# Kernel tuning notes

Hardware: AMD Instinct MI355X
Metric: run time of the kernel (lower is better)

The kernel has to match this reference:

```python
import jax, jax.numpy as jnp
import numpy as np

B, N_PER, H, EMB, V, S, L = 128, 205, 200, 768, 50265, 512, 6
N = B * N_PER

def conv1d(x, w, b, pad):
    # x: [B, Cin, L], w: [Cout, Cin, K]
    out = jax.lax.conv_general_dilated(x, w, (1,), [(pad, pad)],
                                       dimension_numbers=('NCH', 'OIH', 'NCH'))
    return out + b[None, :, None]

def setup_inputs() -> dict:
    key = jax.random.key(0)
    ks = jax.random.split(key, 24)
    s = lambda fan: 1.0 / np.sqrt(fan)
    inp = {
        'x': jax.random.normal(ks[0], (N, H), jnp.float32),
        'edge_index': jax.random.randint(ks[1], (2, 209920), 0, N, jnp.int32),
        'input_ids': jax.random.randint(ks[2], (B, S), 0, V, jnp.int32),
        'embed_table': jax.random.normal(ks[3], (V, EMB), jnp.float32) * 0.02,
        'ggc_w': jax.random.normal(ks[4], (L, H, H), jnp.float32) * s(H),
        'gru_wih': jax.random.normal(ks[5], (3 * H, H), jnp.float32) * s(H),
        'gru_whh': jax.random.normal(ks[6], (3 * H, H), jnp.float32) * s(H),
        'gru_bih': jnp.zeros((3 * H,), jnp.float32),
        'gru_bhh': jnp.zeros((3 * H,), jnp.float32),
        'conv0_w': jax.random.normal(ks[7], (200, 200, 3), jnp.float32) * s(200 * 3),
        'conv0_b': jnp.zeros((200,), jnp.float32),
        'conv1_w': jax.random.normal(ks[8], (200, EMB, 3), jnp.float32) * s(EMB * 3),
        'conv1_b': jnp.zeros((200,), jnp.float32),
        'conv2_w': jax.random.normal(ks[9], (200, EMB, 4), jnp.float32) * s(EMB * 4),
        'conv2_b': jnp.zeros((200,), jnp.float32),
        'conv3_w': jax.random.normal(ks[10], (200, EMB, 5), jnp.float32) * s(EMB * 5),
        'conv3_b': jnp.zeros((200,), jnp.float32),
        'fc1_w': jax.random.normal(ks[11], (256, 800), jnp.float32) * s(800),
        'fc1_b': jnp.zeros((256,), jnp.float32),
        'fc2_w': jax.random.normal(ks[12], (128, 256), jnp.float32) * s(256),
        'fc2_b': jnp.zeros((128,), jnp.float32),
        'fc3_w': jax.random.normal(ks[13], (2, 128), jnp.float32) * s(128),
        'fc3_b': jnp.zeros((2,), jnp.float32),
    }
    return inp

def gated_graph_conv(x, edge_index, ggc_w, wih, whh, bih, bhh):
    src, dst = edge_index[0], edge_index[1]
    h = x  # [N, H], in_dim == out_channels so no padding needed
    for i in range(L):
        m = h @ ggc_w[i]                                   # [N, H]
        agg = jax.ops.segment_sum(m[src], dst, num_segments=N)  # scatter-add at targets
        gi = agg @ wih.T + bih                             # [N, 3H]
        gh = h @ whh.T + bhh
        ir, iz, inn = jnp.split(gi, 3, axis=1)
        hr, hz, hn = jnp.split(gh, 3, axis=1)
        r = jax.nn.sigmoid(ir + hr)
        z = jax.nn.sigmoid(iz + hz)
        n = jnp.tanh(inn + r * hn)
        h = (1.0 - z) * n + z * h
    return h

def reference(x, edge_index, input_ids, embed_table, ggc_w, gru_wih, gru_whh,
              gru_bih, gru_bhh, conv0_w, conv0_b, conv1_w, conv1_b, conv2_w,
              conv2_b, conv3_w, conv3_b, fc1_w, fc1_b, fc2_w, fc2_b, fc3_w, fc3_b):
    g = gated_graph_conv(x, edge_index, ggc_w, gru_wih, gru_whh, gru_bih, gru_bhh)
    g = g.reshape(B, N_PER, H).transpose(0, 2, 1)          # [B, 200, N_PER]
    e = embed_table[input_ids].transpose(0, 2, 1)          # [B, 768, S]
    x0 = jax.nn.relu(conv1d(g, conv0_w, conv0_b, 1))
    x1 = jax.nn.relu(conv1d(e, conv1_w, conv1_b, 0))
    x2 = jax.nn.relu(conv1d(e, conv2_w, conv2_b, 0))
    x3 = jax.nn.relu(conv1d(e, conv3_w, conv3_b, 0))
    feats = jnp.concatenate([x0.max(axis=2), x1.max(axis=2),
                             x2.max(axis=2), x3.max(axis=2)], axis=1)  # [B, 800]
    h = jax.nn.relu(feats @ fc1_w.T + fc1_b)   # dropout is identity in eval
    h = jax.nn.relu(h @ fc2_w.T + fc2_b)
    return h @ fc3_w.T + fc3_b                 # [B, 2]
```

## Files before the change

### kernel.cpp

```cpp
#include <hip/hip_runtime.h>
#include <math.h>

namespace {

constexpr int NB    = 128;
constexpr int NPER  = 205;
constexpr int H     = 200;
constexpr int EMBD  = 768;
constexpr int SEQ   = 512;
constexpr int NLAY  = 6;
constexpr int NNODE = NB * NPER;
constexpr int NEDGE = 209920;
constexpr int KP    = 448;
constexpr int HOFF  = 224;

typedef __bf16 bf16;
typedef _Float16 f16;
typedef __attribute__((ext_vector_type(8))) __bf16 bf16x8;
typedef __attribute__((ext_vector_type(8))) _Float16 f16x8;
typedef __attribute__((ext_vector_type(4))) float f32x4;
typedef unsigned short ushort8 __attribute__((ext_vector_type(8)));
typedef float float4v __attribute__((ext_vector_type(4)));

__device__ __forceinline__ float sigm(float x) { return 1.0f / (1.0f + expf(-x)); }

__device__ __forceinline__ unsigned short f2bf(float x) {
    unsigned int u = __float_as_uint(x);
    unsigned int r = (u + 0x7fffu + ((u >> 16) & 1u)) >> 16;
    return (unsigned short)r;
}
__device__ __forceinline__ unsigned short f2h(float x) {
    union { f16 h; unsigned short u; } c;
    c.h = (f16)x;
    return c.u;
}
__device__ __forceinline__ float h2f(unsigned short u) {
    union { unsigned short u; f16 h; } c;
    c.u = u;
    return (float)c.h;
}

__device__ __forceinline__ int pk_unit(int row, int s) {
    int q = row >> 1;
    return q * 8 + ((((row & 1) << 2) | s) ^ (q & 7));
}

template<bool BIAS, bool OUTF16>
__global__ __launch_bounds__(256, 4)
void gemm_w64(const unsigned short* __restrict__ A, int lda,
              const unsigned short* __restrict__ B, size_t strideBz,
              const float* __restrict__ bias, int Mreal, int Nreal,
              float* __restrict__ Cf, unsigned short* __restrict__ Ch, size_t strideCz,
              int ldc, int Kpad)
{
    __shared__ unsigned short As[128 * 64];
    __shared__ unsigned short Bs[128 * 64];

    const int p0 = blockIdx.x * 128;
    const int o0 = blockIdx.y * 128;
    const unsigned short* Bz = B + (size_t)blockIdx.z * strideBz;
    const int tid = threadIdx.x, lane = tid & 63, wid = tid >> 6;
    const int wm = wid >> 1, wn = wid & 1;
    const int lrow = lane & 15, lk = lane >> 4;

    f32x4 acc[4][4];
    #pragma unroll
    for (int i = 0; i < 4; ++i)
        #pragma unroll
        for (int j = 0; j < 4; ++j) acc[i][j] = (f32x4){0.f, 0.f, 0.f, 0.f};

    for (int c0 = 0; c0 < Kpad; c0 += 64) {
        __syncthreads();
        for (int i = wid; i < 32; i += 4) {
            if (i < 16) {
                int u = i * 64 + lane;
                int row = u >> 3, slot = u & 7;
                int ss = slot ^ (row & 7);
                const unsigned short* sA = A + (size_t)(p0 + row) * lda + c0 + ss * 8;
                __builtin_amdgcn_global_load_lds(
                    (const __attribute__((address_space(1))) void*)sA,
                    (__attribute__((address_space(3))) void*)(As + i * 512), 16, 0, 0);
            } else {
                int i2 = i - 16;
                int u = i2 * 64 + lane;
                int row = u >> 3, slot = u & 7;
                int ss = slot ^ (row & 7);
                const unsigned short* sB = Bz + (size_t)(o0 + row) * Kpad + c0 + ss * 8;
                __builtin_amdgcn_global_load_lds(
                    (const __attribute__((address_space(1))) void*)sB,
                    (__attribute__((address_space(3))) void*)(Bs + i2 * 512), 16, 0, 0);
            }
        }
        __syncthreads();
        #pragma unroll
        for (int hf = 0; hf < 2; ++hf) {
            f16x8 vb[4];
            #pragma unroll
            for (int fn = 0; fn < 4; ++fn) {
                int r = wn * 64 + fn * 16 + lrow;
                int sl = (hf * 4 + lk) ^ (r & 7);
                vb[fn] = *reinterpret_cast<const f16x8*>(&Bs[r * 64 + sl * 8]);
            }
            #pragma unroll
            for (int fm = 0; fm < 4; ++fm) {
                int r = wm * 64 + fm * 16 + lrow;
                int sl = (hf * 4 + lk) ^ (r & 7);
                f16x8 va = *reinterpret_cast<const f16x8*>(&As[r * 64 + sl * 8]);
                #pragma unroll
                for (int fn = 0; fn < 4; ++fn)
                    acc[fm][fn] = __builtin_amdgcn_mfma_f32_16x16x32_f16(va, vb[fn], acc[fm][fn], 0, 0, 0);
            }
        }
    }
    #pragma unroll
    for (int fn = 0; fn < 4; ++fn) {
        int o = o0 + wn * 64 + fn * 16 + lrow;
        if (o >= Nreal) continue;
        float bv = BIAS ? bias[o] : 0.0f;
        #pragma unroll
        for (int fm = 0; fm < 4; ++fm) {
            #pragma unroll
            for (int i = 0; i < 4; ++i) {
                int p = p0 + wm * 64 + fm * 16 + lk * 4 + i;
                if (p >= Mreal) continue;
                float v = acc[fm][fn][i] + bv;
                if (OUTF16) Ch[(size_t)blockIdx.z * strideCz + (size_t)p * ldc + o] = f2h(v);
                else        Cf[(size_t)blockIdx.z * strideCz + (size_t)p * ldc + o] = v;
            }
        }
    }
}

__global__ __launch_bounds__(256, 2)
void gemm_gru(const unsigned short* __restrict__ A,
              const unsigned short* __restrict__ B,
              const float* __restrict__ bb,
              unsigned short* __restrict__ Hn)
{
    __shared__ unsigned short As[2][128 * 64];
    __shared__ unsigned short Bs[2][128 * 64];

    const int p0 = blockIdx.x * 128;
    const int o0 = blockIdx.y * 128;
    const int tid = threadIdx.x, lane = tid & 63, wid = tid >> 6;
    const int wm = wid >> 1, wn = wid & 1;
    const int lrow = lane & 15, lk = lane >> 4;

    auto stage = [&](int bs, int c0) {
        for (int i = wid; i < 32; i += 4) {
            if (i < 16) {
                int u = i * 64 + lane;
                int row = u >> 3, slot = u & 7;
                int ss = slot ^ (row & 7);
                const unsigned short* sA = A + (size_t)(p0 + row) * KP + c0 + ss * 8;
                __builtin_amdgcn_global_load_lds(
                    (const __attribute__((address_space(1))) void*)sA,
                    (__attribute__((address_space(3))) void*)(&As[bs][i * 512]), 16, 0, 0);
            } else {
                int i2 = i - 16;
                int u = i2 * 64 + lane;
                int row = u >> 3, slot = u & 7;
                int ss = slot ^ (row & 7);
                const unsigned short* sB = B + (size_t)(o0 + row) * KP + c0 + ss * 8;
                __builtin_amdgcn_global_load_lds(
                    (const __attribute__((address_space(1))) void*)sB,
                    (__attribute__((address_space(3))) void*)(&Bs[bs][i2 * 512]), 16, 0, 0);
            }
        }
    };

    f32x4 acc[4][4];
    #pragma unroll
    for (int i = 0; i < 4; ++i)
        #pragma unroll
        for (int j = 0; j < 4; ++j) acc[i][j] = (f32x4){0.f, 0.f, 0.f, 0.f};

    stage(0, 0);
    __syncthreads();
    int bs = 0;
    constexpr int NIT = KP / 64;
    for (int t = 0; t < NIT; ++t) {
        if (t + 1 < NIT) stage(bs ^ 1, (t + 1) * 64);
        const unsigned short* Asc = As[bs];
        const unsigned short* Bsc = Bs[bs];
        #pragma unroll
        for (int hf = 0; hf < 2; ++hf) {
            f16x8 vb[4];
            #pragma unroll
            for (int fn = 0; fn < 4; ++fn) {
                int r = wn * 64 + fn * 16 + lrow;
                int sl = (hf * 4 + lk) ^ (r & 7);
                vb[fn] = *reinterpret_cast<const f16x8*>(&Bsc[r * 64 + sl * 8]);
            }
            #pragma unroll
            for (int fm = 0; fm < 4; ++fm) {
                int r = wm * 64 + fm * 16 + lrow;
                int sl = (hf * 4 + lk) ^ (r & 7);
                f16x8 va = *reinterpret_cast<const f16x8*>(&Asc[r * 64 + sl * 8]);
                #pragma unroll
                for (int fn = 0; fn < 4; ++fn)
                    acc[fm][fn] = __builtin_amdgcn_mfma_f32_16x16x32_f16(va, vb[fn], acc[fm][fn], 0, 0, 0);
            }
        }
        __syncthreads();
        bs ^= 1;
    }

    const int colbase = o0 + wn * 64;
    const int c = (colbase >> 2) + lrow;
    float b0 = bb[colbase + 0 * 16 + lrow];
    float b1 = bb[colbase + 1 * 16 + lrow];
    float b2 = bb[colbase + 2 * 16 + lrow];
    float b3 = bb[colbase + 3 * 16 + lrow];
    #pragma unroll
    for (int fm = 0; fm < 4; ++fm) {
        #pragma unroll
        for (int i = 0; i < 4; ++i) {
            int p = p0 + wm * 64 + fm * 16 + lk * 4 + i;
            if (c < H) {
                size_t hidx = (size_t)p * KP + HOFF + c;
                float r = sigm(acc[fm][0][i] + b0);
                float z = sigm(acc[fm][1][i] + b1);
                float nn = tanhf((acc[fm][2][i] + b2) + r * (acc[fm][3][i] + b3));
                float ho = h2f(A[hidx]);
                Hn[hidx] = f2h((1.0f - z) * nn + z * ho);
            }
        }
    }
}

template<int K, int CINP, int LIN, int LOUT>
__global__ __launch_bounds__(512, 4)
void conv_w64(const unsigned short* __restrict__ E, const unsigned short* __restrict__ WT,
              const float* __restrict__ bias, int COUT,
              float* __restrict__ feats, int foff)
{
    constexpr int AROWS  = 272;
    constexpr int AINSTR = AROWS * 4 / 64;
    constexpr int BINSTR = K * 128 * 4 / 64;
    __shared__ unsigned short As[AROWS * 32];
    __shared__ unsigned short Bs[K * 128 * 32];

    const int p0 = blockIdx.x * 256;
    const int o0 = blockIdx.y * 128;
    const int b  = blockIdx.z;
    const int tid = threadIdx.x, lane = tid & 63, wid = tid >> 6;
    const int wm = wid >> 1, wn = wid & 1;
    const int lrow = lane & 15, lk = lane >> 4;

    const unsigned short* Eb = E + (size_t)b * LIN * CINP;

    f32x4 acc[4][4];
    #pragma unroll
    for (int i = 0; i < 4; ++i)
        #pragma unroll
        for (int j = 0; j < 4; ++j) acc[i][j] = (f32x4){0.f, 0.f, 0.f, 0.f};

    for (int c0 = 0; c0 < CINP; c0 += 32) {
        __syncthreads();
        for (int i = wid; i < AINSTR + BINSTR; i += 8) {
            if (i < AINSTR) {
                int u = i * 64 + lane;
                int q = u >> 3, cs = u & 7;
                int bsw = cs ^ (q & 7);
                int row = q * 2 + (bsw >> 2), s = bsw & 3;
                int srow = p0 + row; if (srow > LIN - 1) srow = LIN - 1;
                const unsigned short* src = Eb + (size_t)srow * CINP + c0 + s * 8;
                __builtin_amdgcn_global_load_lds(
                    (const __attribute__((address_space(1))) void*)src,
                    (__attribute__((address_space(3))) void*)(As + i * 512), 16, 0, 0);
            } else {
                int i2 = i - AINSTR;
                int u = i2 * 64 + lane;
                int q = u >> 3, cs = u & 7;
                int bsw = cs ^ (q & 7);
                int R = q * 2 + (bsw >> 2), s = bsw & 3;
                int k = R >> 7, r = R & 127;
                const unsigned short* src = WT + ((size_t)k * 256 + o0 + r) * CINP + c0 + s * 8;
                __builtin_amdgcn_global_load_lds(
                    (const __attribute__((address_space(1))) void*)src,
                    (__attribute__((address_space(3))) void*)(Bs + i2 * 512), 16, 0, 0);
            }
        }
        __syncthreads();
        #pragma unroll
        for (int k = 0; k < K; ++k) {
            bf16x8 vb[4];
            #pragma unroll
            for (int fn = 0; fn < 4; ++fn) {
                int R = k * 128 + wn * 64 + fn * 16 + lrow;
                vb[fn] = *reinterpret_cast<const bf16x8*>(&Bs[pk_unit(R, lk) * 8]);
            }
            #pragma unroll
            for (int fm = 0; fm < 4; ++fm) {
                int r = wm * 64 + fm * 16 + lrow + k;
                bf16x8 va = *reinterpret_cast<const bf16x8*>(&As[pk_unit(r, lk) * 8]);
                #pragma unroll
                for (int fn = 0; fn < 4; ++fn)
                    acc[fm][fn] = __builtin_amdgcn_mfma_f32_16x16x32_bf16(va, vb[fn], acc[fm][fn], 0, 0, 0);
            }
        }
    }
    #pragma unroll
    for (int fn = 0; fn < 4; ++fn) {
        int o = o0 + wn * 64 + fn * 16 + lrow;
        float mx = 0.0f;
        if (o < COUT) {
            float bv = bias[o];
            #pragma unroll
            for (int fm = 0; fm < 4; ++fm)
                #pragma unroll
                for (int i = 0; i < 4; ++i) {
                    int p = p0 + wm * 64 + fm * 16 + lk * 4 + i;
                    if (p < LOUT) mx = fmaxf(mx, acc[fm][fn][i] + bv);
                }
        }
        mx = fmaxf(mx, __shfl_xor(mx, 16));
        mx = fmaxf(mx, __shfl_xor(mx, 32));
        if (lane < 16 && o < COUT)
            atomicMax((int*)&feats[(size_t)b * 800 + foff + o], __float_as_int(mx));
    }
}

__global__ void hist_kernel(const int* __restrict__ dst, int* __restrict__ deg)
{
    int e = blockIdx.x * 256 + threadIdx.x;
    if (e < NEDGE) atomicAdd(&deg[dst[e]], 1);
}

__global__ void scan_kernel(const int* __restrict__ deg, int* __restrict__ off, int* __restrict__ cur)
{
    __shared__ int part[1024];
    const int tid = threadIdx.x;
    const int CH = (NNODE + 1023) / 1024;
    int base = tid * CH;
    int s = 0;
    for (int i = 0; i < CH; ++i) { int idx = base + i; s += (idx < NNODE ? deg[idx] : 0); }
    part[tid] = s;
    __syncthreads();
    for (int d = 1; d < 1024; d <<= 1) {
        int v = (tid >= d) ? part[tid - d] : 0;
        __syncthreads();
        part[tid] += v;
        __syncthreads();
    }
    int run = tid ? part[tid - 1] : 0;
    for (int i = 0; i < CH; ++i) {
        int idx = base + i;
        if (idx < NNODE) { off[idx] = run; cur[idx] = run; run += deg[idx]; }
    }
    if (tid == 1023) off[NNODE] = run;
}

__global__ void fill_kernel(const int* __restrict__ src, const int* __restrict__ dst,
                            int* __restrict__ cur, int* __restrict__ eidx)
{
    int e = blockIdx.x * 256 + threadIdx.x;
    if (e >= NEDGE) return;
    int d = dst[e];
    int pos = atomicAdd(&cur[d], 1);
    eidx[pos] = src[e];
}

__global__ void gather_h2(const int* __restrict__ off, const int* __restrict__ eidx,
                          unsigned short* __restrict__ acat)
{
    int t = blockIdx.x * 256 + threadIdx.x;
    if (t >= NNODE * 32) return;
    int c8 = t & 31, n = t >> 5;
    if (c8 >= 25) return;
    const size_t cb = (size_t)c8 * 8;
    float s[8] = {0.f, 0.f, 0.f, 0.f, 0.f, 0.f, 0.f, 0.f};
    int beg = off[n], end = off[n + 1];
    int i = beg;
    for (; i + 4 <= end; i += 4) {
        int s0 = eidx[i], s1 = eidx[i + 1], s2 = eidx[i + 2], s3 = eidx[i + 3];
        ushort8 a = *(const ushort8*)(acat + (size_t)s0 * KP + HOFF + cb);
        ushort8 b = *(const ushort8*)(acat + (size_t)s1 * KP + HOFF + cb);
        ushort8 c = *(const ushort8*)(acat + (size_t)s2 * KP + HOFF + cb);
        ushort8 d = *(const ushort8*)(acat + (size_t)s3 * KP + HOFF + cb);
        #pragma unroll
        for (int j = 0; j < 8; ++j)
            s[j] += (h2f(a[j]) + h2f(b[j])) + (h2f(c[j]) + h2f(d[j]));
    }
    for (; i < end; ++i) {
        int sn = eidx[i];
        ushort8 hh = *(const ushort8*)(acat + (size_t)sn * KP + HOFF + cb);
        #pragma unroll
        for (int j = 0; j < 8; ++j) s[j] += h2f(hh[j]);
    }
    ushort8 o;
    #pragma unroll
    for (int j = 0; j < 8; ++j) o[j] = f2h(s[j]);
    *(ushort8*)(acat + (size_t)n * KP + cb) = o;
}

__global__ void h0_kernel(const float* __restrict__ x, unsigned short* __restrict__ acat)
{
    int t = blockIdx.x * 256 + threadIdx.x;
    if (t >= NNODE * 32) return;
    int c8 = t & 31, n = t >> 5;
    if (c8 >= 28) return;
    ushort8 o = {0,0,0,0,0,0,0,0};
    if (c8 < 25) {
        const float* src = x + (size_t)n * H + c8 * 8;
        float4v v0 = *(const float4v*)src;
        float4v v1 = *(const float4v*)(src + 4);
        o[0] = f2h(v0[0]); o[1] = f2h(v0[1]); o[2] = f2h(v0[2]); o[3] = f2h(v0[3]);
        o[4] = f2h(v1[0]); o[5] = f2h(v1[1]); o[6] = f2h(v1[2]); o[7] = f2h(v1[3]);
    }
    *(ushort8*)(acat + (size_t)n * KP + HOFF + c8 * 8) = o;
}

__global__ void wih16p_prep(const float* __restrict__ wih, unsigned short* __restrict__ w16)
{
    int t = blockIdx.x * 256 + threadIdx.x;
    if (t >= 896 * 32) return;
    int c8 = t & 31, r = t >> 5;
    int g = (r >> 4) & 3;
    int c = (r >> 6) * 16 + (r & 15);
    ushort8 o = {0,0,0,0,0,0,0,0};
    if (g < 3 && c < H) {
        #pragma unroll
        for (int j = 0; j < 8; ++j) {
            int k = c8 * 8 + j;
            if (k < H) o[j] = f2h(wih[(size_t)(g * 200 + c) * H + k]);
        }
    }
    *(ushort8*)(w16 + (size_t)r * 256 + c8 * 8) = o;
}

__global__ void wl_prep(const float* __restrict__ w, unsigned short* __restrict__ wl)
{
    int t = blockIdx.x * 256 + threadIdx.x;
    if (t >= NLAY * 256 * 32) return;
    int c8 = t & 31;
    int rest = t >> 5;
    int jr = rest & 255;
    int l = rest >> 8;
    ushort8 o = {0,0,0,0,0,0,0,0};
    if (jr < H) {
        #pragma unroll
        for (int j = 0; j < 8; ++j) {
            int k = c8 * 8 + j;
            if (k < H) o[j] = f2h(w[(size_t)l * H * H + (size_t)jr * H + k]);
        }
    }
    *(ushort8*)(wl + (size_t)l * 65536 + (size_t)jr * 256 + c8 * 8) = o;
}

__global__ void wf_rightp(const float* __restrict__ whh, const float* __restrict__ bih,
                          const float* __restrict__ bhh,
                          unsigned short* __restrict__ Wf, float* __restrict__ bb)
{
    int t = blockIdx.x * 256 + threadIdx.x;
    if (t >= NLAY * 896 * 28) return;
    int c8 = t % 28;
    int rest = t / 28;
    int r = rest % 896;
    int l = rest / 896;
    int g = (r >> 4) & 3;
    int c = (r >> 6) * 16 + (r & 15);
    ushort8 o = {0,0,0,0,0,0,0,0};
    if (c < H) {
        #pragma unroll
        for (int j = 0; j < 8; ++j) {
            int kk = c8 * 8 + j;
            float v = 0.0f;
            if (kk < H) {
                if (g == 0)      v = whh[(size_t)c * H + kk];
                else if (g == 1) v = whh[(size_t)(200 + c) * H + kk];
                else if (g == 3) v = whh[(size_t)(400 + c) * H + kk];
            }
            o[j] = f2h(v);
        }
    }
    *(ushort8*)(Wf + (size_t)l * (896 * KP) + (size_t)r * KP + HOFF + c8 * 8) = o;
    if (l == 0 && c8 == 0) {
        float bv = 0.0f;
        if (c < H) {
            if (g == 0)      bv = bih[c] + bhh[c];
            else if (g == 1) bv = bih[200 + c] + bhh[200 + c];
            else if (g == 2) bv = bih[400 + c];
            else             bv = bhh[400 + c];
        }
        bb[r] = bv;
    }
}

__global__ void embed_bf16_kernel(const int* __restrict__ ids, const float* __restrict__ table,
                                  unsigned short* __restrict__ e)
{
    int t = blockIdx.x * 256 + threadIdx.x;
    const int total = NB * SEQ * (EMBD / 8);
    if (t >= total) return;
    int j = t % (EMBD / 8), row = t / (EMBD / 8);
    int id = ids[row];
    const float* src = table + (size_t)id * EMBD + j * 8;
    float4v v0 = *(const float4v*)src;
    float4v v1 = *(const float4v*)(src + 4);
    ushort8 o;
    o[0] = f2bf(v0[0]); o[1] = f2bf(v0[1]); o[2] = f2bf(v0[2]); o[3] = f2bf(v0[3]);
    o[4] = f2bf(v1[0]); o[5] = f2bf(v1[1]); o[6] = f2bf(v1[2]); o[7] = f2bf(v1[3]);
    *(ushort8*)(e + (size_t)row * EMBD + j * 8) = o;
}

__global__ void h_pad_from_acat(const unsigned short* __restrict__ acat,
                                unsigned short* __restrict__ e0)
{
    int t = blockIdx.x * 256 + threadIdx.x;
    const int total = NB * 208 * 32;
    if (t >= total) return;
    int c8 = t % 32, rest = t / 32;
    int r = rest % 208, b = rest / 208;
    ushort8 o = {0,0,0,0,0,0,0,0};
    if (r >= 1 && r <= 205 && c8 < 25) {
        int node = b * NPER + (r - 1);
        ushort8 hh = *(const ushort8*)(acat + (size_t)node * KP + HOFF + c8 * 8);
        #pragma unroll
        for (int j = 0; j < 8; ++j) o[j] = f2bf(h2f(hh[j]));
    }
    *(ushort8*)(e0 + ((size_t)(b * 208 + r)) * 256 + c8 * 8) = o;
}

__global__ void wconv_bf16_kernel(const float* __restrict__ w, unsigned short* __restrict__ wt,
                                  int K, int CINP, int CINR, int COUT)
{
    long long t = (long long)blockIdx.x * 256 + threadIdx.x;
    long long total = (long long)K * 256 * CINP;
    if (t >= total) return;
    int cin = (int)(t % CINP);
    long long rest = t / CINP;
    int o = (int)(rest % 256), k = (int)(rest / 256);
    float v = 0.0f;
    if (o < COUT && cin < CINR) v = w[((size_t)o * CINR + cin) * K + k];
    wt[t] = f2bf(v);
}

__global__ __launch_bounds__(256)
void fc_head(const float* __restrict__ feats,
             const float* __restrict__ w1, const float* __restrict__ b1,
             const float* __restrict__ w2, const float* __restrict__ b2,
             const float* __restrict__ w3, const float* __restrict__ b3,
             float* __restrict__ out)
{
    __shared__ float f[800];
    __shared__ float h1[256];
    __shared__ float h2[128];
    const int b = blockIdx.x, tid = threadIdx.x;
    for (int i = tid; i < 800; i += 256) f[i] = feats[(size_t)b * 800 + i];
    __syncthreads();
    {
        float acc = b1[tid];
        const float* wr = w1 + (size_t)tid * 800;
        for (int k = 0; k < 800; ++k) acc = fmaf(f[k], wr[k], acc);
        h1[tid] = fmaxf(acc, 0.0f);
    }
    __syncthreads();
    if (tid < 128) {
        float acc = b2[tid];
        const float* wr = w2 + (size_t)tid * 256;
        for (int k = 0; k < 256; ++k) acc = fmaf(h1[k], wr[k], acc);
        h2[tid] = fmaxf(acc, 0.0f);
    }
    __syncthreads();
    if (tid < 2) {
        float acc = b3[tid];
        const float* wr = w3 + (size_t)tid * 128;
        for (int k = 0; k < 128; ++k) acc = fmaf(h2[k], wr[k], acc);
        out[(size_t)b * 2 + tid] = acc;
    }
}

}

extern "C" void kernel_launch(void* const* d_in, const int* in_sizes, int n_in,
                              void* d_out, int out_size, void* d_ws, size_t ws_size,
                              hipStream_t stream)
{
    const float* x         = (const float*)d_in[0];
    const int*   edge      = (const int*)d_in[1];
    const int*   input_ids = (const int*)d_in[2];
    const float* table     = (const float*)d_in[3];
    const float* ggc_w     = (const float*)d_in[4];
    const float* wih       = (const float*)d_in[5];
    const float* whh       = (const float*)d_in[6];
    const float* bih       = (const float*)d_in[7];
    const float* bhh       = (const float*)d_in[8];
    const float* c0w = (const float*)d_in[9];  const float* c0b = (const float*)d_in[10];
    const float* c1w = (const float*)d_in[11]; const float* c1b = (const float*)d_in[12];
    const float* c2w = (const float*)d_in[13]; const float* c2b = (const float*)d_in[14];
    const float* c3w = (const float*)d_in[15]; const float* c3b = (const float*)d_in[16];
    const float* f1w = (const float*)d_in[17]; const float* f1b = (const float*)d_in[18];
    const float* f2w = (const float*)d_in[19]; const float* f2b = (const float*)d_in[20];
    const float* f3w = (const float*)d_in[21]; const float* f3b = (const float*)d_in[22];
    float* out = (float*)d_out;

    float* ws = (float*)d_ws;
    unsigned short* acat_a = (unsigned short*)(ws + 0);
    unsigned short* acat_b = (unsigned short*)(ws + 5877760);
    unsigned short* Wf     = (unsigned short*)(ws + 11755520);
    unsigned short* wl16   = (unsigned short*)(ws + 12959744);
    unsigned short* wih16p = (unsigned short*)(ws + 13156352);
    float* b_big = ws + 13271040;
    int* deg  = (int*)(ws + 13271936);
    int* off  = (int*)(ws + 13298176);
    int* cur  = (int*)(ws + 13324417);
    int* eidx = (int*)(ws + 13350658);
    unsigned short* e_bf16 = (unsigned short*)(ws + 0);
    unsigned short* e0     = (unsigned short*)(ws + 25165824);
    unsigned short* wt0    = (unsigned short*)(ws + 28600000);
    unsigned short* wt1    = wt0 + (size_t)3 * 256 * 256;
    unsigned short* wt2    = wt1 + (size_t)3 * 256 * EMBD;
    unsigned short* wt3    = wt2 + (size_t)4 * 256 * EMBD;
    float* feats = ws + 29900000;

    const int* srcp = edge;
    const int* dstp = edge + NEDGE;

    dim3 blk(256);
    dim3 blk512(512);

    hipMemsetAsync(deg, 0, sizeof(int) * NNODE, stream);
    hist_kernel<<<dim3((NEDGE + 255) / 256), blk, 0, stream>>>(dstp, deg);
    scan_kernel<<<dim3(1), dim3(1024), 0, stream>>>(deg, off, cur);
    fill_kernel<<<dim3((NEDGE + 255) / 256), blk, 0, stream>>>(srcp, dstp, cur, eidx);
    h0_kernel<<<dim3((NNODE * 32 + 255) / 256), blk, 0, stream>>>(x, acat_a);
    wih16p_prep<<<dim3((896 * 32 + 255) / 256), blk, 0, stream>>>(wih, wih16p);
    wl_prep<<<dim3((NLAY * 256 * 32 + 255) / 256), blk, 0, stream>>>(ggc_w, wl16);
    hipMemsetAsync(Wf, 0, (size_t)NLAY * 896 * KP * 2, stream);
    wf_rightp<<<dim3((NLAY * 896 * 28 + 255) / 256), blk, 0, stream>>>(whh, bih, bhh, Wf, b_big);
    gemm_w64<false, true><<<dim3(7, 2, NLAY), blk, 0, stream>>>(
        wih16p, 256, wl16, (size_t)256 * 256, nullptr, 896, 200,
        nullptr, Wf, (size_t)896 * KP, KP, 256);

    unsigned short* bufs[2] = { acat_a, acat_b };
    for (int l = 0; l < NLAY; ++l) {
        unsigned short* curb = bufs[l & 1];
        unsigned short* nxtb = bufs[(l + 1) & 1];
        gather_h2<<<dim3((NNODE * 32 + 255) / 256), blk, 0, stream>>>(off, eidx, curb);
        gemm_gru<<<dim3(NNODE / 128, 7), blk, 0, stream>>>(
            curb, Wf + (size_t)l * (896 * KP), b_big, nxtb);
    }

    h_pad_from_acat<<<dim3((NB * 208 * 32 + 255) / 256), blk, 0, stream>>>(acat_a, e0);
    embed_bf16_kernel<<<dim3(NB * SEQ * (EMBD / 8) / 256), blk, 0, stream>>>(input_ids, table, e_bf16);
    wconv_bf16_kernel<<<dim3((3 * 256 * 256 + 255) / 256), blk, 0, stream>>>(c0w, wt0, 3, 256, 200, 200);
    wconv_bf16_kernel<<<dim3((3 * 256 * EMBD + 255) / 256), blk, 0, stream>>>(c1w, wt1, 3, EMBD, EMBD, 200);
    wconv_bf16_kernel<<<dim3((4 * 256 * EMBD + 255) / 256), blk, 0, stream>>>(c2w, wt2, 4, EMBD, EMBD, 200);
    wconv_bf16_kernel<<<dim3((5 * 256 * EMBD + 255) / 256), blk, 0, stream>>>(c3w, wt3, 5, EMBD, EMBD, 200);

    hipMemsetAsync(feats, 0, sizeof(float) * NB * 800, stream);
    conv_w64<3, 256, 208, 205><<<dim3(1, 2, NB), blk512, 0, stream>>>(e0, wt0, c0b, 200, feats, 0);
    conv_w64<3, EMBD, SEQ, 510><<<dim3(2, 2, NB), blk512, 0, stream>>>(e_bf16, wt1, c1b, 200, feats, 200);
    conv_w64<4, EMBD, SEQ, 509><<<dim3(2, 2, NB), blk512, 0, stream>>>(e_bf16, wt2, c2b, 200, feats, 400);
    conv_w64<5, EMBD, SEQ, 508><<<dim3(2, 2, NB), blk512, 0, stream>>>(e_bf16, wt3, c3b, 200, feats, 600);

    fc_head<<<dim3(NB), blk, 0, stream>>>(feats, f1w, f1b, f2w, f2b, f3w, f3b, out);
}
```

Before: 905.1 us.

## Restructure conv kernel: weights in registers, double-buffered LDS input tiles

The conv kernel now loads its weight fragments straight from global memory into registers instead of staging them in LDS. It also double-buffers the activation tile in LDS, prefetching the next channel chunk while MFMAs run on the current one, with explicit vmcnt waits and barriers. Tiles shrink to 128 positions with 256-thread blocks, so more blocks are launched. The aim is to overlap memory with compute and to cut LDS traffic and syncs, at the cost of higher register pressure (K*4 bf16x8 weight vectors live per thread) and hand-tuned waitcnt correctness.

```diff
diff --git a/kernel.cpp b/kernel.cpp
--- a/kernel.cpp
+++ b/kernel.cpp
@@ -43,6 +43,13 @@
 __device__ __forceinline__ int pk_unit(int row, int s) {
     int q = row >> 1;
     return q * 8 + ((((row & 1) << 2) | s) ^ (q & 7));
+}
+
+template<int N> __device__ __forceinline__ void waitcnt_vm() {
+    if constexpr (N == 12)      asm volatile("s_waitcnt vmcnt(12)" ::: "memory");
+    else if constexpr (N == 16) asm volatile("s_waitcnt vmcnt(16)" ::: "memory");
+    else if constexpr (N == 20) asm volatile("s_waitcnt vmcnt(20)" ::: "memory");
+    else                        asm volatile("s_waitcnt vmcnt(0)"  ::: "memory");
 }
 
 template<bool BIAS, bool OUTF16>
@@ -230,18 +237,16 @@
 }
 
 template<int K, int CINP, int LIN, int LOUT>
-__global__ __launch_bounds__(512, 4)
-void conv_w64(const unsigned short* __restrict__ E, const unsigned short* __restrict__ WT,
-              const float* __restrict__ bias, int COUT,
-              float* __restrict__ feats, int foff)
-{
-    constexpr int AROWS  = 272;
+__global__ __launch_bounds__(256, (K >= 4 ? 2 : 3))
+void conv_breg(const unsigned short* __restrict__ E, const unsigned short* __restrict__ WT,
+               const float* __restrict__ bias, int COUT,
+               float* __restrict__ feats, int foff)
+{
+    constexpr int AROWS  = 144;
     constexpr int AINSTR = AROWS * 4 / 64;
-    constexpr int BINSTR = K * 128 * 4 / 64;
-    __shared__ unsigned short As[AROWS * 32];
-    __shared__ unsigned short Bs[K * 128 * 32];
-
-    const int p0 = blockIdx.x * 256;
+    __shared__ unsigned short As[2][AROWS * 32];
+
+    const int p0 = blockIdx.x * 128;
     const int o0 = blockIdx.y * 128;
     const int b  = blockIdx.z;
     const int tid = threadIdx.x, lane = tid & 63, wid = tid >> 6;
@@ -249,6 +254,22 @@
     const int lrow = lane & 15, lk = lane >> 4;
 
     const unsigned short* Eb = E + (size_t)b * LIN * CINP;
+    const unsigned short* Wl = WT + ((size_t)(o0 + wn * 64 + lrow)) * CINP + lk * 8;
+
+    auto stageA = [&](int bufsel, int c0) {
+        #pragma unroll
+        for (int i = wid; i < AINSTR; i += 4) {
+            int u = i * 64 + lane;
+            int q = u >> 3, cs = u & 7;
+            int bsw = cs ^ (q & 7);
+            int row = q * 2 + (bsw >> 2), s = bsw & 3;
+            int srow = p0 + row; if (srow > LIN - 1) srow = LIN - 1;
+            const unsigned short* src = Eb + (size_t)srow * CINP + c0 + s * 8;
+            __builtin_amdgcn_global_load_lds(
+                (const __attribute__((address_space(1))) void*)src,
+                (__attribute__((address_space(3))) void*)(&As[bufsel][i * 512]), 16, 0, 0);
+        }
+    };
 
     f32x4 acc[4][4];
     #pragma unroll
@@ -256,51 +277,55 @@
         #pragma unroll
         for (int j = 0; j < 4; ++j) acc[i][j] = (f32x4){0.f, 0.f, 0.f, 0.f};
 
-    for (int c0 = 0; c0 < CINP; c0 += 32) {
-        __syncthreads();
-        for (int i = wid; i < AINSTR + BINSTR; i += 8) {
-            if (i < AINSTR) {
-                int u = i * 64 + lane;
-                int q = u >> 3, cs = u & 7;
-                int bsw = cs ^ (q & 7);
-                int row = q * 2 + (bsw >> 2), s = bsw & 3;
-                int srow = p0 + row; if (srow > LIN - 1) srow = LIN - 1;
-                const unsigned short* src = Eb + (size_t)srow * CINP + c0 + s * 8;
-                __builtin_amdgcn_global_load_lds(
-                    (const __attribute__((address_space(1))) void*)src,
-                    (__attribute__((address_space(3))) void*)(As + i * 512), 16, 0, 0);
-            } else {
-                int i2 = i - AINSTR;
-                int u = i2 * 64 + lane;
-                int q = u >> 3, cs = u & 7;
-                int bsw = cs ^ (q & 7);
-                int R = q * 2 + (bsw >> 2), s = bsw & 3;
-                int k = R >> 7, r = R & 127;
-                const unsigned short* src = WT + ((size_t)k * 256 + o0 + r) * CINP + c0 + s * 8;
-                __builtin_amdgcn_global_load_lds(
-                    (const __attribute__((address_space(1))) void*)src,
-                    (__attribute__((address_space(3))) void*)(Bs + i2 * 512), 16, 0, 0);
-            }
-        }
-        __syncthreads();
+    bf16x8 vb[K][4];
+
+    stageA(0, 0);
+    #pragma unroll
+    for (int k = 0; k < K; ++k)
+        #pragma unroll
+        for (int fn = 0; fn < 4; ++fn)
+            vb[k][fn] = *reinterpret_cast<const bf16x8*>(Wl + ((size_t)(k * 256 + fn * 16)) * CINP);
+    waitcnt_vm<4 * K>();
+    __builtin_amdgcn_sched_barrier(0);
+    __builtin_amdgcn_s_barrier();
+    __builtin_amdgcn_sched_barrier(0);
+
+    constexpr int nit = CINP / 32;
+    int buf = 0;
+    for (int t = 0; t < nit; ++t) {
+        const bool pf = (t + 1 < nit);
+        if (pf) stageA(buf ^ 1, (t + 1) * 32);
+        const unsigned short* Asc = As[buf];
+        const int cnext = (t + 1) * 32;
         #pragma unroll
         for (int k = 0; k < K; ++k) {
-            bf16x8 vb[4];
-            #pragma unroll
-            for (int fn = 0; fn < 4; ++fn) {
-                int R = k * 128 + wn * 64 + fn * 16 + lrow;
-                vb[fn] = *reinterpret_cast<const bf16x8*>(&Bs[pk_unit(R, lk) * 8]);
-            }
+            bf16x8 va[4];
             #pragma unroll
             for (int fm = 0; fm < 4; ++fm) {
                 int r = wm * 64 + fm * 16 + lrow + k;
-                bf16x8 va = *reinterpret_cast<const bf16x8*>(&As[pk_unit(r, lk) * 8]);
+                va[fm] = *reinterpret_cast<const bf16x8*>(&Asc[pk_unit(r, lk) * 8]);
+            }
+            #pragma unroll
+            for (int fm = 0; fm < 4; ++fm)
                 #pragma unroll
                 for (int fn = 0; fn < 4; ++fn)
-                    acc[fm][fn] = __builtin_amdgcn_mfma_f32_16x16x32_bf16(va, vb[fn], acc[fm][fn], 0, 0, 0);
-            }
-        }
-    }
+                    acc[fm][fn] = __builtin_amdgcn_mfma_f32_16x16x32_bf16(va[fm], vb[k][fn], acc[fm][fn], 0, 0, 0);
+            if (pf) {
+                #pragma unroll
+                for (int fn = 0; fn < 4; ++fn)
+                    vb[k][fn] = *reinterpret_cast<const bf16x8*>(
+                        Wl + ((size_t)(k * 256 + fn * 16)) * CINP + cnext);
+            }
+        }
+        if (pf) {
+            waitcnt_vm<4 * K>();
+            __builtin_amdgcn_sched_barrier(0);
+            __builtin_amdgcn_s_barrier();
+            __builtin_amdgcn_sched_barrier(0);
+        }
+        buf ^= 1;
+    }
+
     #pragma unroll
     for (int fn = 0; fn < 4; ++fn) {
         int o = o0 + wn * 64 + fn * 16 + lrow;
@@ -619,7 +644,6 @@
     const int* dstp = edge + NEDGE;
 
     dim3 blk(256);
-    dim3 blk512(512);
 
     hipMemsetAsync(deg, 0, sizeof(int) * NNODE, stream);
     hist_kernel<<<dim3((NEDGE + 255) / 256), blk, 0, stream>>>(dstp, deg);
@@ -651,10 +675,10 @@
     wconv_bf16_kernel<<<dim3((5 * 256 * EMBD + 255) / 256), blk, 0, stream>>>(c3w, wt3, 5, EMBD, EMBD, 200);
 
     hipMemsetAsync(feats, 0, sizeof(float) * NB * 800, stream);
-    conv_w64<3, 256, 208, 205><<<dim3(1, 2, NB), blk512, 0, stream>>>(e0, wt0, c0b, 200, feats, 0);
-    conv_w64<3, EMBD, SEQ, 510><<<dim3(2, 2, NB), blk512, 0, stream>>>(e_bf16, wt1, c1b, 200, feats, 200);
-    conv_w64<4, EMBD, SEQ, 509><<<dim3(2, 2, NB), blk512, 0, stream>>>(e_bf16, wt2, c2b, 200, feats, 400);
-    conv_w64<5, EMBD, SEQ, 508><<<dim3(2, 2, NB), blk512, 0, stream>>>(e_bf16, wt3, c3b, 200, feats, 600);
+    conv_breg<3, 256, 208, 205><<<dim3(2, 2, NB), blk, 0, stream>>>(e0, wt0, c0b, 200, feats, 0);
+    conv_breg<3, EMBD, SEQ, 510><<<dim3(4, 2, NB), blk, 0, stream>>>(e_bf16, wt1, c1b, 200, feats, 200);
+    conv_breg<4, EMBD, SEQ, 509><<<dim3(4, 2, NB), blk, 0, stream>>>(e_bf16, wt2, c2b, 200, feats, 400);
+    conv_breg<5, EMBD, SEQ, 508><<<dim3(4, 2, NB), blk, 0, stream>>>(e_bf16, wt3, c3b, 200, feats, 600);
 
     fc_head<<<dim3(NB), blk, 0, stream>>>(feats, f1w, f1b, f2w, f2b, f3w, f3b, out);
 }
```

Measured after the change: 1.250 ms. 38.1% more time.
